# Kernel optimization log

Hardware: AMD Instinct MI355X
Metric: run time of the kernel (lower is better)

## Reference

```python
import jax, jax.numpy as jnp
import numpy as np

N_NODES = 100000
N_EDGES = 1600000
NEG_SLOPE = 0.2
EPS = 1e-16


def gat_conv(x, edge_index, W, att_src, att_dst, bias, heads, out_ch, concat):
    # x: [N, F_in]; edge_index: [2, E] with edge (src j -> dst i)
    N = x.shape[0]
    src, dst = edge_index[0], edge_index[1]
    h = (x @ W).reshape(N, heads, out_ch)              # [N, H, C]
    a_src = (h * att_src[None]).sum(-1)                # [N, H]
    a_dst = (h * att_dst[None]).sum(-1)                # [N, H]
    e = a_src[src] + a_dst[dst]                        # [E, H]
    e = jnp.where(e > 0, e, NEG_SLOPE * e)             # LeakyReLU(0.2)
    # segment softmax over destination node
    m = jax.ops.segment_max(e, dst, num_segments=N)    # [N, H]
    m = jnp.where(jnp.isfinite(m), m, 0.0)
    ex = jnp.exp(e - m[dst])                           # [E, H]
    s = jax.ops.segment_sum(ex, dst, num_segments=N)   # [N, H]
    alpha = ex / (s[dst] + EPS)                        # [E, H]
    msg = h[src] * alpha[..., None]                    # [E, H, C]
    out = jax.ops.segment_sum(msg, dst, num_segments=N)  # [N, H, C]
    if concat:
        out = out.reshape(N, heads * out_ch)
    else:
        out = out.mean(axis=1)
    return out + bias


def setup_inputs() -> dict:
    key = jax.random.key(0)
    ks = jax.random.split(key, 8)
    x = jax.random.normal(ks[0], (N_NODES, 2), dtype=jnp.float32)
    edge_index = jax.random.randint(ks[1], (2, N_EDGES), 0, N_NODES, dtype=jnp.int64)
    glorot = lambda k, shape, fan: jax.random.normal(k, shape, jnp.float32) * (1.0 / np.sqrt(fan))
    W1 = glorot(ks[2], (2, 128), 2)
    att_src1 = glorot(ks[3], (8, 16), 16)
    att_dst1 = glorot(ks[4], (8, 16), 16)
    b1 = jnp.zeros((128,), jnp.float32)
    W2 = glorot(ks[5], (128, 4), 128)
    att_src2 = glorot(ks[6], (1, 4), 4)
    att_dst2 = glorot(ks[7], (1, 4), 4)
    b2 = jnp.zeros((4,), jnp.float32)
    return {"x": x, "edge_index": edge_index, "W1": W1, "att_src1": att_src1,
            "att_dst1": att_dst1, "b1": b1, "W2": W2, "att_src2": att_src2,
            "att_dst2": att_dst2, "b2": b2}


def reference(x, edge_index, W1, att_src1, att_dst1, b1, W2, att_src2, att_dst2, b2):
    h = gat_conv(x, edge_index, W1, att_src1, att_dst1, b1, heads=8, out_ch=16, concat=True)
    h = jax.nn.relu(h)
    # dropout p=0.6 is identity in eval mode
    h = gat_conv(h, edge_index, W2, att_src2, att_dst2, b2, heads=1, out_ch=4, concat=True)
    return jax.nn.log_softmax(h, axis=1)
```

## Files before the change

### kernel.cpp

```cpp
#include <hip/hip_runtime.h>
#include <math.h>

static constexpr float kNegSlope = 0.2f;
static constexpr float kEps = 1e-16f;
static constexpr int SLICES = 256;
static constexpr int BSHIFT = 7;
static constexpr int BMASK = 127;
static constexpr unsigned SRCMASK = 0x1FFFFu;
static constexpr int CAP = 2816;

__device__ __forceinline__ float leaky(float v) {
    return v > 0.0f ? v : kNegSlope * v;
}


__global__ __launch_bounds__(512) void k_hist1(const int* __restrict__ ei,
                                               int* __restrict__ table,
                                               int* __restrict__ rowptr,
                                               int E, int N, int NBUCK) {
    __shared__ int hist[832];
    int b = blockIdx.x, t = threadIdx.x;
    if (b == 0 && t == 0) rowptr[N] = E;
    for (int i = t; i < NBUCK; i += 512) hist[i] = 0;
    __syncthreads();
    int S = (((E + SLICES - 1) / SLICES) + 3) & ~3;
    int lo = b * S, hi = min(lo + S, E);
    for (int i = lo + t * 4; i < hi; i += 512 * 4) {
        int4 dv = *(const int4*)(ei + E + i);
        atomicAdd(&hist[dv.x >> BSHIFT], 1);
        atomicAdd(&hist[dv.y >> BSHIFT], 1);
        atomicAdd(&hist[dv.z >> BSHIFT], 1);
        atomicAdd(&hist[dv.w >> BSHIFT], 1);
    }
    __syncthreads();
    for (int i = t; i < NBUCK; i += 512) table[i * SLICES + b] = hist[i];
}

__global__ __launch_bounds__(256) void k_scan_reduce(const int* __restrict__ src,
                                                     int* __restrict__ partial, int n) {
    __shared__ int wsum[4];
    int b = blockIdx.x, t = threadIdx.x;
    int base = b * 1024 + t * 4;
    int s = 0;
#pragma unroll
    for (int k = 0; k < 4; ++k) {
        int idx = base + k;
        s += (idx < n) ? src[idx] : 0;
    }
#pragma unroll
    for (int off = 1; off < 64; off <<= 1) s += __shfl_xor(s, off);
    if ((t & 63) == 0) wsum[t >> 6] = s;
    __syncthreads();
    if (t == 0) partial[b] = wsum[0] + wsum[1] + wsum[2] + wsum[3];
}

__global__ __launch_bounds__(256) void k_scan_apply(int* __restrict__ data,
                                                    const int* __restrict__ partial,
                                                    int n, int nsb) {
    __shared__ int sm[8];
    __shared__ int baseSh;
    int b = blockIdx.x, t = threadIdx.x;
    int acc = 0;
    for (int i = t; i < b; i += 256) acc += partial[i];
#pragma unroll
    for (int off = 1; off < 64; off <<= 1) acc += __shfl_xor(acc, off);
    if ((t & 63) == 0) sm[t >> 6] = acc;
    __syncthreads();
    if (t == 0) baseSh = sm[0] + sm[1] + sm[2] + sm[3];
    __syncthreads();
    int chunkBase = baseSh;
    __syncthreads();
    int base = b * 1024 + t * 4;
    int v[4];
#pragma unroll
    for (int k = 0; k < 4; ++k) {
        int idx = base + k;
        v[k] = (idx < n) ? data[idx] : 0;
    }
    int sum4 = v[0] + v[1] + v[2] + v[3];
    int s = sum4;
#pragma unroll
    for (int off = 1; off < 64; off <<= 1) {
        int u = __shfl_up(s, off);
        if ((t & 63) >= off) s += u;
    }
    if ((t & 63) == 63) sm[t >> 6] = s;
    __syncthreads();
    int woff = 0;
    int w = t >> 6;
    for (int ww = 0; ww < w; ++ww) woff += sm[ww];
    int ex = chunkBase + woff + (s - sum4);
#pragma unroll
    for (int k = 0; k < 4; ++k) {
        int idx = base + k;
        if (idx < n) data[idx] = ex;
        ex += v[k];
    }
}

__global__ __launch_bounds__(512) void k_bin2(const int* __restrict__ ei,
                                              const int* __restrict__ table,
                                              unsigned* __restrict__ sbuf, int E, int NBUCK) {
    __shared__ int cur[832];
    int b = blockIdx.x, t = threadIdx.x;
    for (int i = t; i < NBUCK; i += 512) cur[i] = table[i * SLICES + b];
    __syncthreads();
    int S = (((E + SLICES - 1) / SLICES) + 3) & ~3;
    int lo = b * S, hi = min(lo + S, E);
    for (int i = lo + t * 4; i < hi; i += 512 * 4) {
        int4 sv = *(const int4*)(ei + i);
        int4 dv = *(const int4*)(ei + E + i);
        int pos;
        pos = atomicAdd(&cur[dv.x >> BSHIFT], 1);
        sbuf[pos] = (unsigned)sv.x | ((unsigned)(dv.x & BMASK) << 17);
        pos = atomicAdd(&cur[dv.y >> BSHIFT], 1);
        sbuf[pos] = (unsigned)sv.y | ((unsigned)(dv.y & BMASK) << 17);
        pos = atomicAdd(&cur[dv.z >> BSHIFT], 1);
        sbuf[pos] = (unsigned)sv.z | ((unsigned)(dv.z & BMASK) << 17);
        pos = atomicAdd(&cur[dv.w >> BSHIFT], 1);
        sbuf[pos] = (unsigned)sv.w | ((unsigned)(dv.w & BMASK) << 17);
    }
}

__global__ __launch_bounds__(512) void k_sort(
        const unsigned* __restrict__ sbuf, const int* __restrict__ table,
        int* __restrict__ rowptr, int* __restrict__ ssrc,
        int N, int E, int NBUCK) {
    __shared__ int hist[128];
    __shared__ int sc[128];
    __shared__ int cur[128];
    __shared__ unsigned raws[CAP];
    __shared__ int sls[CAP];
    int b = blockIdx.x;
    int t = threadIdx.x;
    int lo = table[b * SLICES];
    int hi = (b + 1 < NBUCK) ? table[(b + 1) * SLICES] : E;
    int cnt = hi - lo;
    bool inLds = (cnt <= CAP);

    if (t < 128) hist[t] = 0;
    __syncthreads();

    if (inLds) {
        for (int i = t; i < cnt; i += 512) {
            unsigned v = sbuf[lo + i];
            raws[i] = v;
            atomicAdd(&hist[v >> 17], 1);
        }
    } else {
        for (int i = lo + t; i < hi; i += 512) atomicAdd(&hist[sbuf[i] >> 17], 1);
    }
    __syncthreads();

    if (t < 128) {
        int lane = t & 63;
        int own = hist[t];
        int v = own;
#pragma unroll
        for (int off = 1; off < 64; off <<= 1) {
            int u = __shfl_up(v, off);
            if (lane >= off) v += u;
        }
        sc[t] = v;
    }
    __syncthreads();
    if (t < 128) {
        int ex = sc[t] - hist[t] + (t >= 64 ? sc[63] : 0);
        cur[t] = ex;
        int node = (b << BSHIFT) + t;
        if (node < N) rowptr[node] = lo + ex;
    }
    __syncthreads();

    if (inLds) {
        for (int i = t; i < cnt; i += 512) {
            unsigned v = raws[i];
            int pos = atomicAdd(&cur[v >> 17], 1);
            sls[pos] = (int)(v & SRCMASK);
        }
        __syncthreads();
        for (int i = t; i < cnt; i += 512) ssrc[lo + i] = sls[i];
    } else {
        for (int i = lo + t; i < hi; i += 512) {
            unsigned v = sbuf[i];
            int pos = atomicAdd(&cur[v >> 17], 1);
            ssrc[lo + pos] = (int)(v & SRCMASK);
        }
    }
}

__global__ __launch_bounds__(256) void k_gather1(
        const int* __restrict__ rowptr, const int* __restrict__ ssrc,
        const float* __restrict__ x,
        const float* __restrict__ W1, const float* __restrict__ att_src1,
        const float* __restrict__ att_dst1,
        float* __restrict__ attA, float* __restrict__ attB, int N) {
    __shared__ float pbuf[32];
    int t = threadIdx.x;
    if (t < 32) {
        int which = t >> 4;
        int hd = t & 15;
        int h = hd >> 1, d = hd & 1;
        const float* att = which ? att_dst1 : att_src1;
        float s = 0.0f;
#pragma unroll
        for (int c = 0; c < 16; ++c) s += W1[d * 128 + h * 16 + c] * att[h * 16 + c];
        pbuf[which * 16 + d * 8 + h] = s;
    }
    __syncthreads();

    int idx = blockIdx.x * blockDim.x + t;
    int n = idx >> 3, q = idx & 7;
    if (n >= N) return;
    const float2* x2 = (const float2*)x;
    int start = rowptr[n], end = rowptr[n + 1];
    float2 xn = x2[n];
    float Ps0[8], Ps1[8], adv[8], l[8], s0[8], s1[8];
#pragma unroll
    for (int h = 0; h < 8; ++h) {
        Ps0[h] = pbuf[h];
        Ps1[h] = pbuf[8 + h];
        adv[h] = xn.x * pbuf[16 + h] + xn.y * pbuf[24 + h];
        l[h] = 0.f; s0[h] = 0.f; s1[h] = 0.f;
    }
    int j = start + q;
    for (; j + 8 < end; j += 16) {
        int sa = ssrc[j];
        int sb = ssrc[j + 8];
        float2 xa = x2[sa];
        float2 xb = x2[sb];
#pragma unroll
        for (int h = 0; h < 8; ++h) {
            float pa = __expf(leaky(xa.x * Ps0[h] + xa.y * Ps1[h] + adv[h]));
            float pb = __expf(leaky(xb.x * Ps0[h] + xb.y * Ps1[h] + adv[h]));
            l[h] += pa + pb;
            s0[h] += pa * xa.x + pb * xb.x;
            s1[h] += pa * xa.y + pb * xb.y;
        }
    }
    if (j < end) {
        int sa = ssrc[j];
        float2 xa = x2[sa];
#pragma unroll
        for (int h = 0; h < 8; ++h) {
            float pa = __expf(leaky(xa.x * Ps0[h] + xa.y * Ps1[h] + adv[h]));
            l[h] += pa;
            s0[h] += pa * xa.x;
            s1[h] += pa * xa.y;
        }
    }
#pragma unroll
    for (int off = 1; off < 8; off <<= 1) {
#pragma unroll
        for (int h = 0; h < 8; ++h) {
            l[h] += __shfl_xor(l[h], off);
            s0[h] += __shfl_xor(s0[h], off);
            s1[h] += __shfl_xor(s1[h], off);
        }
    }
    float inv = 1.0f / (l[q] + kEps);
    attA[n * 8 + q] = s0[q] * inv;
    attB[n * 8 + q] = s1[q] * inv;
}

__global__ __launch_bounds__(256) void k_fold(
        const float* __restrict__ attA, const float* __restrict__ attB,
        const float* __restrict__ W1, const float* __restrict__ b1,
        const float* __restrict__ W2, float* __restrict__ h2, int N) {
    __shared__ float4 pk1[128];
    __shared__ float4 pk2[128];
    int t = threadIdx.x;
    if (t < 128) {
        pk1[t] = make_float4(W1[t], W1[128 + t], b1[t], 0.f);
        pk2[t] = ((const float4*)W2)[t];
    }
    __syncthreads();
    int n = blockIdx.x * 256 + t;
    if (n >= N) return;
    const float4* A = (const float4*)(attA + n * 8);
    const float4* B = (const float4*)(attB + n * 8);
    float4 a01 = A[0], a23 = A[1];
    float4 b01 = B[0], b23 = B[1];
    float4 acc = make_float4(0.f, 0.f, 0.f, 0.f);
#pragma unroll
    for (int h = 0; h < 8; ++h) {
        float sx0 = (h == 0) ? a01.x : (h == 1) ? a01.y : (h == 2) ? a01.z :
                    (h == 3) ? a01.w : (h == 4) ? a23.x : (h == 5) ? a23.y :
                    (h == 6) ? a23.z : a23.w;
        float sx1 = (h == 0) ? b01.x : (h == 1) ? b01.y : (h == 2) ? b01.z :
                    (h == 3) ? b01.w : (h == 4) ? b23.x : (h == 5) ? b23.y :
                    (h == 6) ? b23.z : b23.w;
#pragma unroll
        for (int c = 0; c < 16; ++c) {
            int col = h * 16 + c;
            float4 p = pk1[col];
            float o = fmaxf(p.x * sx0 + p.y * sx1 + p.z, 0.0f);
            float4 w = pk2[col];
            acc.x += o * w.x;
            acc.y += o * w.y;
            acc.z += o * w.z;
            acc.w += o * w.w;
        }
    }
    ((float4*)h2)[n] = acc;
}

__global__ __launch_bounds__(256) void k_gather2_out(
        const int* __restrict__ rowptr, const int* __restrict__ ssrc,
        const float* __restrict__ h2, const float* __restrict__ att_src2,
        const float* __restrict__ att_dst2, const float* __restrict__ b2,
        float* __restrict__ out, int N) {
    int idx = blockIdx.x * blockDim.x + threadIdx.x;
    int n = idx >> 3, q = idx & 7;
    if (n >= N) return;
    int start = rowptr[n], end = rowptr[n + 1];
    float4 as2 = *(const float4*)att_src2;
    float4 ad2v = *(const float4*)att_dst2;
    const float4* h4 = (const float4*)h2;
    float4 hn = h4[n];
    float ad = hn.x * ad2v.x + hn.y * ad2v.y + hn.z * ad2v.z + hn.w * ad2v.w;
    float l = 0.0f;
    float4 acc = make_float4(0.f, 0.f, 0.f, 0.f);
    int j = start + q;
    for (; j + 8 < end; j += 16) {
        int s0 = ssrc[j];
        int s1 = ssrc[j + 8];
        float4 ha = h4[s0];
        float4 hb = h4[s1];
        float e0 = ha.x * as2.x + ha.y * as2.y + ha.z * as2.z + ha.w * as2.w + ad;
        float e1 = hb.x * as2.x + hb.y * as2.y + hb.z * as2.z + hb.w * as2.w + ad;
        float p0 = __expf(leaky(e0));
        float p1 = __expf(leaky(e1));
        l += p0 + p1;
        acc.x += p0 * ha.x + p1 * hb.x;
        acc.y += p0 * ha.y + p1 * hb.y;
        acc.z += p0 * ha.z + p1 * hb.z;
        acc.w += p0 * ha.w + p1 * hb.w;
    }
    if (j < end) {
        int s0 = ssrc[j];
        float4 ha = h4[s0];
        float e0 = ha.x * as2.x + ha.y * as2.y + ha.z * as2.z + ha.w * as2.w + ad;
        float p0 = __expf(leaky(e0));
        l += p0;
        acc.x += p0 * ha.x;
        acc.y += p0 * ha.y;
        acc.z += p0 * ha.z;
        acc.w += p0 * ha.w;
    }
#pragma unroll
    for (int off = 1; off < 8; off <<= 1) {
        l += __shfl_xor(l, off);
        acc.x += __shfl_xor(acc.x, off);
        acc.y += __shfl_xor(acc.y, off);
        acc.z += __shfl_xor(acc.z, off);
        acc.w += __shfl_xor(acc.w, off);
    }
    if (q == 0) {
        float inv = 1.0f / (l + kEps);
        float4 v = make_float4(acc.x * inv + b2[0], acc.y * inv + b2[1],
                               acc.z * inv + b2[2], acc.w * inv + b2[3]);
        float mx = fmaxf(fmaxf(v.x, v.y), fmaxf(v.z, v.w));
        float sum = __expf(v.x - mx) + __expf(v.y - mx) + __expf(v.z - mx) + __expf(v.w - mx);
        float lse = mx + logf(sum);
        ((float4*)out)[n] = make_float4(v.x - lse, v.y - lse, v.z - lse, v.w - lse);
    }
}

extern "C" void kernel_launch(void* const* d_in, const int* in_sizes, int n_in,
                              void* d_out, int out_size, void* d_ws, size_t ws_size,
                              hipStream_t stream) {
    const float* x        = (const float*)d_in[0];
    const int*   ei       = (const int*)d_in[1];
    const float* W1       = (const float*)d_in[2];
    const float* att_src1 = (const float*)d_in[3];
    const float* att_dst1 = (const float*)d_in[4];
    const float* b1       = (const float*)d_in[5];
    const float* W2       = (const float*)d_in[6];
    const float* att_src2 = (const float*)d_in[7];
    const float* att_dst2 = (const float*)d_in[8];
    const float* b2       = (const float*)d_in[9];

    const int N = in_sizes[0] / 2;
    const int E = in_sizes[1] / 2;
    const int NBUCK = (N + BMASK) >> BSHIFT;
    const int ntable = NBUCK * SLICES;
    const int nsb = (ntable + 1023) / 1024;

    int* table     = (int*)d_ws;
    int* partial   = table + ntable + 64;
    int* rowptr    = partial + 1024;
    int* ssrc      = rowptr + ((N + 4) & ~3);
    unsigned* sbuf = (unsigned*)(ssrc + E);
    float* attA    = (float*)sbuf;
    float* attB    = attA + (size_t)N * 8;
    size_t post    = (size_t)E > (size_t)N * 16 ? (size_t)E : (size_t)N * 16;
    float* h2      = (float*)(sbuf + post);

    k_hist1<<<SLICES, 512, 0, stream>>>(ei, table, rowptr, E, N, NBUCK);
    k_scan_reduce<<<nsb, 256, 0, stream>>>(table, partial, ntable);
    k_scan_apply<<<nsb, 256, 0, stream>>>(table, partial, ntable, nsb);
    k_bin2<<<SLICES, 512, 0, stream>>>(ei, table, sbuf, E, NBUCK);

    k_sort<<<NBUCK, 512, 0, stream>>>(sbuf, table, rowptr, ssrc, N, E, NBUCK);

    k_gather1<<<(N * 8 + 255) / 256, 256, 0, stream>>>(rowptr, ssrc, x,
                                                       W1, att_src1, att_dst1,
                                                       attA, attB, N);
    k_fold<<<(N + 255) / 256, 256, 0, stream>>>(attA, attB, W1, b1, W2, h2, N);

    k_gather2_out<<<(N * 8 + 255) / 256, 256, 0, stream>>>(rowptr, ssrc, h2,
                                                           att_src2, att_dst2, b2,
                                                           (float*)d_out, N);
}
```

Measured before the change: 151.2 us.

## Split layer-1 gather work per head across 16 lanes per node

```diff
diff --git a/kernel.cpp b/kernel.cpp
--- a/kernel.cpp
+++ b/kernel.cpp
@@ -210,57 +210,46 @@
     __syncthreads();
 
     int idx = blockIdx.x * blockDim.x + t;
-    int n = idx >> 3, q = idx & 7;
+    int n = idx >> 4;
+    int sub = idx & 15;
+    int h = sub & 7;
+    int p = sub >> 3;
     if (n >= N) return;
     const float2* x2 = (const float2*)x;
     int start = rowptr[n], end = rowptr[n + 1];
     float2 xn = x2[n];
-    float Ps0[8], Ps1[8], adv[8], l[8], s0[8], s1[8];
-#pragma unroll
-    for (int h = 0; h < 8; ++h) {
-        Ps0[h] = pbuf[h];
-        Ps1[h] = pbuf[8 + h];
-        adv[h] = xn.x * pbuf[16 + h] + xn.y * pbuf[24 + h];
-        l[h] = 0.f; s0[h] = 0.f; s1[h] = 0.f;
-    }
-    int j = start + q;
-    for (; j + 8 < end; j += 16) {
+    float Ps0 = pbuf[h];
+    float Ps1 = pbuf[8 + h];
+    float adv = xn.x * pbuf[16 + h] + xn.y * pbuf[24 + h];
+    float l = 0.f, s0 = 0.f, s1 = 0.f;
+    int j = start + p;
+    for (; j + 2 < end; j += 4) {
         int sa = ssrc[j];
-        int sb = ssrc[j + 8];
+        int sb = ssrc[j + 2];
         float2 xa = x2[sa];
         float2 xb = x2[sb];
-#pragma unroll
-        for (int h = 0; h < 8; ++h) {
-            float pa = __expf(leaky(xa.x * Ps0[h] + xa.y * Ps1[h] + adv[h]));
-            float pb = __expf(leaky(xb.x * Ps0[h] + xb.y * Ps1[h] + adv[h]));
-            l[h] += pa + pb;
-            s0[h] += pa * xa.x + pb * xb.x;
-            s1[h] += pa * xa.y + pb * xb.y;
-        }
+        float pa = __expf(leaky(fmaf(xa.x, Ps0, fmaf(xa.y, Ps1, adv))));
+        float pb = __expf(leaky(fmaf(xb.x, Ps0, fmaf(xb.y, Ps1, adv))));
+        l += pa + pb;
+        s0 = fmaf(pa, xa.x, fmaf(pb, xb.x, s0));
+        s1 = fmaf(pa, xa.y, fmaf(pb, xb.y, s1));
     }
     if (j < end) {
         int sa = ssrc[j];
         float2 xa = x2[sa];
-#pragma unroll
-        for (int h = 0; h < 8; ++h) {
-            float pa = __expf(leaky(xa.x * Ps0[h] + xa.y * Ps1[h] + adv[h]));
-            l[h] += pa;
-            s0[h] += pa * xa.x;
-            s1[h] += pa * xa.y;
-        }
-    }
-#pragma unroll
-    for (int off = 1; off < 8; off <<= 1) {
-#pragma unroll
-        for (int h = 0; h < 8; ++h) {
-            l[h] += __shfl_xor(l[h], off);
-            s0[h] += __shfl_xor(s0[h], off);
-            s1[h] += __shfl_xor(s1[h], off);
-        }
-    }
-    float inv = 1.0f / (l[q] + kEps);
-    attA[n * 8 + q] = s0[q] * inv;
-    attB[n * 8 + q] = s1[q] * inv;
+        float pa = __expf(leaky(fmaf(xa.x, Ps0, fmaf(xa.y, Ps1, adv))));
+        l += pa;
+        s0 = fmaf(pa, xa.x, s0);
+        s1 = fmaf(pa, xa.y, s1);
+    }
+    l += __shfl_xor(l, 8);
+    s0 += __shfl_xor(s0, 8);
+    s1 += __shfl_xor(s1, 8);
+    if (p == 0) {
+        float inv = 1.0f / (l + kEps);
+        attA[n * 8 + h] = s0 * inv;
+        attB[n * 8 + h] = s1 * inv;
+    }
 }
 
 __global__ __launch_bounds__(256) void k_fold(
@@ -404,9 +393,9 @@
 
     k_sort<<<NBUCK, 512, 0, stream>>>(sbuf, table, rowptr, ssrc, N, E, NBUCK);
 
-    k_gather1<<<(N * 8 + 255) / 256, 256, 0, stream>>>(rowptr, ssrc, x,
-                                                       W1, att_src1, att_dst1,
-                                                       attA, attB, N);
+    k_gather1<<<(N * 16 + 255) / 256, 256, 0, stream>>>(rowptr, ssrc, x,
+                                                        W1, att_src1, att_dst1,
+                                                        attA, attB, N);
     k_fold<<<(N + 255) / 256, 256, 0, stream>>>(attA, attB, W1, b1, W2, h2, N);
 
     k_gather2_out<<<(N * 8 + 255) / 256, 256, 0, stream>>>(rowptr, ssrc, h2,
```

Result: no change. 151.6 us (+0.3%).
